# Kernel optimization log

Hardware: AMD Instinct MI355X
Metric: run time of the kernel (lower is better)

Reference implementation:

```python
import jax, jax.numpy as jnp
import numpy as np

GROUPS = 32
EPS = 1e-5


def _group_norm(x, w, b):
    B, C, H, W = x.shape
    xr = x.reshape(B, GROUPS, C // GROUPS, H, W)
    mean = xr.mean(axis=(2, 3, 4), keepdims=True)
    var = xr.var(axis=(2, 3, 4), keepdims=True)
    xn = ((xr - mean) * jax.lax.rsqrt(var + EPS)).reshape(B, C, H, W)
    return xn * w[None, :, None, None] + b[None, :, None, None]


def _conv1x1(w, b, x):
    # 1x1 conv == per-pixel channel matmul
    return jnp.einsum('oc,bchw->bohw', w, x) + b[None, :, None, None]


def setup_inputs() -> dict:
    key = jax.random.key(0)
    ks = jax.random.split(key, 6)
    C = 512
    s = 1.0 / np.sqrt(C)  # kaiming-uniform-ish scale for 1x1 convs
    return {
        'x': jax.random.normal(ks[0], (4, C, 64, 64), jnp.float32),
        'gn_w': jnp.ones((C,), jnp.float32),
        'gn_b': jnp.zeros((C,), jnp.float32),
        'qw': jax.random.normal(ks[1], (C, C), jnp.float32) * s,
        'qb': jnp.zeros((C,), jnp.float32),
        'kw': jax.random.normal(ks[2], (C, C), jnp.float32) * s,
        'kb': jnp.zeros((C,), jnp.float32),
        'vw': jax.random.normal(ks[3], (C, C), jnp.float32) * s,
        'vb': jnp.zeros((C,), jnp.float32),
        'pw': jax.random.normal(ks[4], (C, C), jnp.float32) * s,
        'pb': jnp.zeros((C,), jnp.float32),
    }


def reference(x, gn_w, gn_b, qw, qb, kw, kb, vw, vb, pw, pb):
    B, C, H, W = x.shape
    h_ = _group_norm(x, gn_w, gn_b)
    q = _conv1x1(qw, qb, h_).reshape(B, C, H * W)
    k = _conv1x1(kw, kb, h_).reshape(B, C, H * W)
    v = _conv1x1(vw, vb, h_).reshape(B, C, H * W)
    # scores [B, HW(query), HW(key)]
    scores = jnp.einsum('bcq,bck->bqk', q, k) * (C ** -0.5)
    attn = jax.nn.softmax(scores, axis=-1)
    out = jnp.einsum('bqk,bdk->bdq', attn, v).reshape(B, C, H, W)
    return x + _conv1x1(pw, pb, out)
```

## Files before the change

### kernel.cpp

```cpp
#include <hip/hip_runtime.h>

#define DEV __device__ __forceinline__

typedef __attribute__((ext_vector_type(8))) short short8;
typedef __attribute__((ext_vector_type(4))) float floatx4;
typedef __attribute__((ext_vector_type(4))) int i32x4;
typedef __attribute__((ext_vector_type(2))) long longx2;

DEV unsigned short f2bs(float x) {
    unsigned u = __float_as_uint(x);
    unsigned r = (u + 0x7fffu + ((u >> 16) & 1u)) >> 16;
    return (unsigned short)r;
}

DEV unsigned char f2fp8(float x) {
#if __has_builtin(__builtin_amdgcn_cvt_pk_fp8_f32)
    int pk = __builtin_amdgcn_cvt_pk_fp8_f32(x, 0.f, 0, false);
    return (unsigned char)(pk & 0xff);
#else
    unsigned u = __float_as_uint(x);
    unsigned s = (u >> 24) & 0x80;
    u &= 0x7fffffff;
    unsigned um = u + 0x7ffff + ((u >> 20) & 1);
    int e = (int)(um >> 23) - 120;
    unsigned char r;
    if (e <= 0) {
        float ax = __uint_as_float(u);
        int q = (int)rintf(ax * 512.f);
        r = (unsigned char)((q > 7) ? 8 : q);
    } else {
        r = (unsigned char)((e << 3) | ((um >> 20) & 7));
    }
    return r | s;
#endif
}

DEV unsigned pack_fp8x4(float v0, float v1, float v2, float v3) {
#if __has_builtin(__builtin_amdgcn_cvt_pk_fp8_f32)
    unsigned pk = (unsigned)__builtin_amdgcn_cvt_pk_fp8_f32(v0, v1, 0, false);
    pk = (unsigned)__builtin_amdgcn_cvt_pk_fp8_f32(v2, v3, (int)pk, true);
    return pk;
#else
    return (unsigned)f2fp8(v0) | ((unsigned)f2fp8(v1) << 8) |
           ((unsigned)f2fp8(v2) << 16) | ((unsigned)f2fp8(v3) << 24);
#endif
}

DEV unsigned pack_i8x4(float v0, float v1, float v2, float v3) {
    unsigned b0 = (unsigned)((int)rintf(v0)) & 255u;
    unsigned b1 = (unsigned)((int)rintf(v1)) & 255u;
    unsigned b2 = (unsigned)((int)rintf(v2)) & 255u;
    unsigned b3 = (unsigned)((int)rintf(v3)) & 255u;
    return b0 | (b1 << 8) | (b2 << 16) | (b3 << 24);
}

__global__ void gn_stats_kernel(const float* __restrict__ x, float* __restrict__ stats,
                                float* __restrict__ rowsum) {
    int bg = blockIdx.x;
    int tid = threadIdx.x;
    if (tid < 128) rowsum[bg * 128 + tid] = 0.f;
    const float4* p = (const float4*)(x + (size_t)bg * 65536);
    float s = 0.f, ss = 0.f;
    for (int i = tid; i < 16384; i += 256) {
        float4 v = p[i];
        s += v.x + v.y + v.z + v.w;
        ss += v.x * v.x + v.y * v.y + v.z * v.z + v.w * v.w;
    }
    for (int off = 32; off; off >>= 1) { s += __shfl_down(s, off); ss += __shfl_down(ss, off); }
    __shared__ float rs[4], rss[4];
    int wave = tid >> 6, lane = tid & 63;
    if (lane == 0) { rs[wave] = s; rss[wave] = ss; }
    __syncthreads();
    if (tid == 0) {
        float S = rs[0] + rs[1] + rs[2] + rs[3];
        float SS = rss[0] + rss[1] + rss[2] + rss[3];
        float mean = S * (1.f / 65536.f);
        float var = SS * (1.f / 65536.f) - mean * mean;
        stats[bg * 2] = mean;
        stats[bg * 2 + 1] = rsqrtf(var + 1e-5f);
    }
}

__global__ void gn_apply_kernel(const float* __restrict__ x, const float* __restrict__ stats,
                                const float* __restrict__ gw, const float* __restrict__ gb,
                                unsigned short* __restrict__ ht) {
    __shared__ __align__(16) unsigned short t[64][72];
    int b = blockIdx.z, c0 = blockIdx.y * 64, p0 = blockIdx.x * 64;
    int tid = threadIdx.x;
    const float* xb = x + ((size_t)b * 512 + c0) * 4096 + p0;
#pragma unroll
    for (int pass = 0; pass < 4; ++pass) {
        int cl = pass * 16 + (tid >> 4);
        int pq = (tid & 15) * 4;
        float4 v = *(const float4*)(xb + (size_t)cl * 4096 + pq);
        int c = c0 + cl, g = c >> 4;
        float mean = stats[(b * 32 + g) * 2], rstd = stats[(b * 32 + g) * 2 + 1];
        float sw = gw[c] * rstd;
        float sb = gb[c] - mean * sw;
        t[pq + 0][cl] = f2bs(v.x * sw + sb);
        t[pq + 1][cl] = f2bs(v.y * sw + sb);
        t[pq + 2][cl] = f2bs(v.z * sw + sb);
        t[pq + 3][cl] = f2bs(v.w * sw + sb);
    }
    __syncthreads();
    unsigned short* hb = ht + ((size_t)b * 4096 + p0) * 512 + c0;
#pragma unroll
    for (int pass = 0; pass < 2; ++pass) {
        int pl = pass * 32 + (tid >> 3);
        int c8 = (tid & 7) * 8;
        *(uint4*)(hb + (size_t)pl * 512 + c8) = *(const uint4*)&t[pl][c8];
    }
}

__global__ void cvt_bf16_kernel(const float* __restrict__ s, unsigned short* __restrict__ d, int n4) {
    int i = blockIdx.x * 256 + threadIdx.x;
    if (i >= n4) return;
    float4 v = ((const float4*)s)[i];
    ushort4 o;
    o.x = f2bs(v.x); o.y = f2bs(v.y); o.z = f2bs(v.z); o.w = f2bs(v.w);
    ((ushort4*)d)[i] = o;
}

template <int EPI>
__global__ void gemm_nt(const unsigned short* __restrict__ A, long long sAb,
                        const unsigned short* __restrict__ B, long long sBb,
                        void* __restrict__ Cv, void* __restrict__ Cv2, long long sCb,
                        const float* __restrict__ bias,
                        const float* __restrict__ resid, long long sRb,
                        int M, int N, int K, int Nst, int NS, float scale) {
    __shared__ __align__(16) unsigned short lA[128 * 64];
    __shared__ __align__(16) unsigned short lB[128 * 64];
    const int tid = threadIdx.x;
    const int wave = tid >> 6, lane = tid & 63;
    const int m0 = blockIdx.y * 128, n0 = blockIdx.x * 128, bz = blockIdx.z;
    const unsigned short* Ab = A + (size_t)bz * sAb;
    const unsigned short* Bb = B + (size_t)bz * sBb;

    floatx4 acc[4][4];
#pragma unroll
    for (int i = 0; i < 4; i++)
#pragma unroll
        for (int j = 0; j < 4; j++) acc[i][j] = (floatx4){0.f, 0.f, 0.f, 0.f};

    const int wm = (wave >> 1) * 64, wn = (wave & 1) * 64;
    const int quad = lane >> 4;
    const int lc = lane & 15;
    const int lc7 = lc & 7;

    const int nk = K >> 6;
    for (int kt = 0; kt < nk; ++kt) {
        const int kbase = kt * 64;
#pragma unroll
        for (int c = 0; c < 4; ++c) {
            int d = c * 256 + tid;
            int r = d >> 3;
            int kc = (d & 7) ^ (r & 7);
            const unsigned short* ga = Ab + (size_t)(m0 + r) * K + kbase + kc * 8;
            const unsigned short* gb = Bb + (size_t)(n0 + r) * K + kbase + kc * 8;
            __builtin_amdgcn_global_load_lds(
                (const __attribute__((address_space(1))) void*)ga,
                (__attribute__((address_space(3))) void*)&lA[(size_t)(c * 256 + wave * 64) * 8], 16, 0, 0);
            __builtin_amdgcn_global_load_lds(
                (const __attribute__((address_space(1))) void*)gb,
                (__attribute__((address_space(3))) void*)&lB[(size_t)(c * 256 + wave * 64) * 8], 16, 0, 0);
        }
        __syncthreads();
#pragma unroll
        for (int kk = 0; kk < 2; ++kk) {
            const int swz = ((kk * 4 + quad) ^ lc7) * 8;
            short8 af[4], bf[4];
#pragma unroll
            for (int i = 0; i < 4; i++)
                af[i] = *(const short8*)&lA[(size_t)(wm + i * 16 + lc) * 64 + swz];
#pragma unroll
            for (int j = 0; j < 4; j++)
                bf[j] = *(const short8*)&lB[(size_t)(wn + j * 16 + lc) * 64 + swz];
#pragma unroll
            for (int i = 0; i < 4; i++)
#pragma unroll
                for (int j = 0; j < 4; j++)
                    acc[i][j] = __builtin_amdgcn_mfma_f32_16x16x32_bf16(af[i], bf[j], acc[i][j], 0, 0, 0);
        }
        __syncthreads();
    }

    const int rowb = quad * 4;
#pragma unroll
    for (int i = 0; i < 4; i++) {
#pragma unroll
        for (int r = 0; r < 4; r++) {
            const int m = m0 + wm + i * 16 + rowb + r;
            if constexpr (EPI == 0) {
                float q[4];
#pragma unroll
                for (int j = 0; j < 4; j++) {
                    const int n = n0 + wn + j * 16 + lc;
                    q[j] = fminf(fmaxf((acc[i][j][r] + bias[n]) * scale, -127.f), 127.f);
                }
                const int col64 = n0 + wn;
                char* outp = (char*)((col64 < NS) ? Cv : Cv2);
                size_t idx = (size_t)bz * sCb + (size_t)m * Nst +
                             (col64 - ((col64 < NS) ? 0 : NS)) + lc * 4;
                *(unsigned*)(outp + idx) = pack_i8x4(q[0], q[1], q[2], q[3]);
            } else if constexpr (EPI == 5) {
                const float bm = bias[m];
                float q[4];
#pragma unroll
                for (int j = 0; j < 4; j++)
                    q[j] = fminf(fmaxf(acc[i][j][r] + bm, -448.f), 448.f);
                size_t idx = (size_t)bz * sCb + (size_t)m * Nst + n0 + wn + lc * 4;
                *(unsigned*)((char*)Cv + idx) = pack_fp8x4(q[0], q[1], q[2], q[3]);
            } else {
#pragma unroll
                for (int j = 0; j < 4; j++) {
                    const int n = n0 + wn + j * 16 + lc;
                    size_t idx = (size_t)bz * sCb + (size_t)m * Nst + n;
                    ((float*)Cv)[idx] = acc[i][j][r] + bias[m] +
                                        resid[(size_t)bz * sRb + (size_t)m * Nst + n];
                }
            }
        }
    }
}

__global__ void gemm_i8_exp(const char* __restrict__ A, long long sAb,
                            const char* __restrict__ B, long long sBb,
                            char* __restrict__ Cv, long long sCb,
                            float* __restrict__ rowsum,
                            int M, int N, int K, float scale2) {
    __shared__ __align__(16) char lA[128 * 128];
    __shared__ __align__(16) char lB[128 * 128];
    const int tid = threadIdx.x;
    const int wave = tid >> 6, lane = tid & 63;
    const int m0 = blockIdx.y * 128, n0 = blockIdx.x * 128, bz = blockIdx.z;
    const char* Ab = A + (size_t)bz * sAb;
    const char* Bb = B + (size_t)bz * sBb;

    i32x4 acc[4][4];
#pragma unroll
    for (int i = 0; i < 4; i++)
#pragma unroll
        for (int j = 0; j < 4; j++) acc[i][j] = (i32x4){0, 0, 0, 0};

    const int wm = (wave >> 1) * 64, wn = (wave & 1) * 64;
    const int quad = lane >> 4;
    const int lc = lane & 15;
    const int lc7 = lc & 7;

    const int nk = K >> 7;
    for (int kt = 0; kt < nk; ++kt) {
        const int kbase = kt * 128;
#pragma unroll
        for (int c = 0; c < 4; ++c) {
            int d = c * 256 + tid;
            int r = d >> 3;
            int kc = (d & 7) ^ (r & 7);
            const char* ga = Ab + (size_t)(m0 + r) * K + kbase + kc * 16;
            const char* gb = Bb + (size_t)(n0 + r) * K + kbase + kc * 16;
            __builtin_amdgcn_global_load_lds(
                (const __attribute__((address_space(1))) void*)ga,
                (__attribute__((address_space(3))) void*)&lA[(size_t)(c * 256 + wave * 64) * 16], 16, 0, 0);
            __builtin_amdgcn_global_load_lds(
                (const __attribute__((address_space(1))) void*)gb,
                (__attribute__((address_space(3))) void*)&lB[(size_t)(c * 256 + wave * 64) * 16], 16, 0, 0);
        }
        __syncthreads();
#pragma unroll
        for (int kk = 0; kk < 2; ++kk) {
            const int swz = ((kk * 4 + quad) ^ lc7) * 16;
            i32x4 af[4], bf[4];
#pragma unroll
            for (int i = 0; i < 4; i++)
                af[i] = *(const i32x4*)&lA[(size_t)(wm + i * 16 + lc) * 128 + swz];
#pragma unroll
            for (int j = 0; j < 4; j++)
                bf[j] = *(const i32x4*)&lB[(size_t)(wn + j * 16 + lc) * 128 + swz];
#pragma unroll
            for (int i = 0; i < 4; i++)
#pragma unroll
                for (int j = 0; j < 4; j++)
                    acc[i][j] = __builtin_amdgcn_mfma_i32_16x16x64_i8(af[i], bf[j], acc[i][j], 0, 0, 0);
        }
        __syncthreads();
    }

    const int rowb = quad * 4;
#pragma unroll
    for (int i = 0; i < 4; i++) {
#pragma unroll
        for (int r = 0; r < 4; r++) {
            const int m = m0 + wm + i * 16 + rowb + r;
            float e[4];
            float rsacc = 0.f;
#pragma unroll
            for (int j = 0; j < 4; j++) {
                e[j] = fminf(exp2f(fmaf((float)acc[i][j][r], scale2, -2.0f)), 448.f);
                rsacc += e[j];
            }
            size_t idx = (size_t)bz * sCb + (size_t)m * N + n0 + wn + lc * 4;
            *(unsigned*)(Cv + idx) = pack_fp8x4(e[0], e[1], e[2], e[3]);
            rsacc += __shfl_xor(rsacc, 1);
            rsacc += __shfl_xor(rsacc, 2);
            rsacc += __shfl_xor(rsacc, 4);
            rsacc += __shfl_xor(rsacc, 8);
            if (lc == 0) atomicAdd(&rowsum[(size_t)bz * M + m], rsacc);
        }
    }
}

__global__ void gemm_fp8_o(const char* __restrict__ A, long long sAb,
                           const char* __restrict__ B, long long sBb,
                           unsigned short* __restrict__ Cv, long long sCb,
                           const float* __restrict__ rowsum,
                           int M, int N, int K) {
    __shared__ __align__(16) char lA[128 * 128];
    __shared__ __align__(16) char lB[128 * 128];
    const int tid = threadIdx.x;
    const int wave = tid >> 6, lane = tid & 63;
    int flat = blockIdx.x;
    int xcd = flat & 7, idx = flat >> 3;
    int nt = idx & 3, si = idx >> 2;
    int stripe = xcd * 16 + si;
    const int m0 = (stripe & 31) * 128;
    const int n0 = nt * 128;
    const int bz = stripe >> 5;
    const char* Ab = A + (size_t)bz * sAb;
    const char* Bb = B + (size_t)bz * sBb;

    floatx4 acc[4][4];
#pragma unroll
    for (int i = 0; i < 4; i++)
#pragma unroll
        for (int j = 0; j < 4; j++) acc[i][j] = (floatx4){0.f, 0.f, 0.f, 0.f};

    const int wm = (wave >> 1) * 64, wn = (wave & 1) * 64;
    const int quad = lane >> 4;
    const int lc = lane & 15;
    const int lc7 = lc & 7;
    const int half = quad & 1;

    const int nk = K >> 7;
    for (int kt = 0; kt < nk; ++kt) {
        const int kbase = kt * 128;
#pragma unroll
        for (int c = 0; c < 4; ++c) {
            int d = c * 256 + tid;
            int r = d >> 3;
            int kc = (d & 7) ^ (r & 7);
            const char* ga = Ab + (size_t)(m0 + r) * K + kbase + kc * 16;
            const char* gb = Bb + (size_t)(n0 + r) * K + kbase + kc * 16;
            __builtin_amdgcn_global_load_lds(
                (const __attribute__((address_space(1))) void*)ga,
                (__attribute__((address_space(3))) void*)&lA[(size_t)(c * 256 + wave * 64) * 16], 16, 0, 0);
            __builtin_amdgcn_global_load_lds(
                (const __attribute__((address_space(1))) void*)gb,
                (__attribute__((address_space(3))) void*)&lB[(size_t)(c * 256 + wave * 64) * 16], 16, 0, 0);
        }
        __syncthreads();
#pragma unroll
        for (int t = 0; t < 4; ++t) {
            const int swz = ((2 * t + (quad >> 1)) ^ lc7) * 16;
            long a8[4], b8[4];
#pragma unroll
            for (int i = 0; i < 4; i++) {
                longx2 v = *(const longx2*)&lA[(size_t)(wm + i * 16 + lc) * 128 + swz];
                a8[i] = v[half];
            }
#pragma unroll
            for (int j = 0; j < 4; j++) {
                longx2 v = *(const longx2*)&lB[(size_t)(wn + j * 16 + lc) * 128 + swz];
                b8[j] = v[half];
            }
#pragma unroll
            for (int i = 0; i < 4; i++)
#pragma unroll
                for (int j = 0; j < 4; j++)
                    acc[i][j] = __builtin_amdgcn_mfma_f32_16x16x32_fp8_fp8(a8[i], b8[j], acc[i][j], 0, 0, 0);
        }
        __syncthreads();
    }

    const int rowb = quad * 4;
#pragma unroll
    for (int i = 0; i < 4; i++) {
#pragma unroll
        for (int r = 0; r < 4; r++) {
            const int m = m0 + wm + i * 16 + rowb + r;
            const float pscale = 1.f / rowsum[(size_t)bz * M + m];
#pragma unroll
            for (int j = 0; j < 4; j++) {
                const int n = n0 + wn + j * 16 + lc;
                Cv[(size_t)bz * sCb + (size_t)m * N + n] = f2bs(acc[i][j][r] * pscale);
            }
        }
    }
}

extern "C" void kernel_launch(void* const* d_in, const int* in_sizes, int n_in,
                              void* d_out, int out_size, void* d_ws, size_t ws_size,
                              hipStream_t stream) {
    (void)in_sizes; (void)n_in; (void)out_size; (void)ws_size;
    const float* x   = (const float*)d_in[0];
    const float* gnw = (const float*)d_in[1];
    const float* gnb = (const float*)d_in[2];
    const float* qw  = (const float*)d_in[3];
    const float* qb  = (const float*)d_in[4];
    const float* kw  = (const float*)d_in[5];
    const float* kb  = (const float*)d_in[6];
    const float* vw  = (const float*)d_in[7];
    const float* vb  = (const float*)d_in[8];
    const float* pw  = (const float*)d_in[9];
    const float* pb  = (const float*)d_in[10];
    float* out = (float*)d_out;

    char* ws = (char*)d_ws;
    unsigned short* h_t = (unsigned short*)(ws);
    unsigned short* o_t = h_t;
    char* q_i8 = (char*)(ws + (16ull << 20));
    char* k_i8 = (char*)(ws + (32ull << 20));
    char* v_f8 = (char*)(ws + (48ull << 20));
    unsigned short* wqkb = (unsigned short*)(ws + (64ull << 20));
    unsigned short* wvb = (unsigned short*)(ws + (65ull << 20));
    unsigned short* wpb = wvb + 262144;
    float* stats  = (float*)(ws + (66ull << 20));
    float* rowsum = (float*)(ws + (66ull << 20) + 65536);
    float* biasqk = (float*)(ws + (66ull << 20) + 131072);
    char* p_f8 = (char*)(ws + (67ull << 20));

    const long long sP  = 2097152;
    const long long sS  = 16777216;
    const int BIG = 1 << 30;
    const float QS = 16.f;
    const float SC = 0.044194173824159216f / (QS * QS);
    const float LOG2E = 1.4426950408889634f;

    cvt_bf16_kernel<<<256, 256, 0, stream>>>(qw, wqkb, 65536);
    cvt_bf16_kernel<<<256, 256, 0, stream>>>(kw, wqkb + 262144, 65536);
    cvt_bf16_kernel<<<256, 256, 0, stream>>>(vw, wvb, 65536);
    cvt_bf16_kernel<<<256, 256, 0, stream>>>(pw, wpb, 65536);
    hipMemcpyAsync(biasqk, qb, 512 * sizeof(float), hipMemcpyDeviceToDevice, stream);
    hipMemcpyAsync(biasqk + 512, kb, 512 * sizeof(float), hipMemcpyDeviceToDevice, stream);
    gn_stats_kernel<<<128, 256, 0, stream>>>(x, stats, rowsum);
    gn_apply_kernel<<<dim3(64, 8, 4), 256, 0, stream>>>(x, stats, gnw, gnb, h_t);
    gemm_nt<0><<<dim3(8, 32, 4), 256, 0, stream>>>(h_t, sP, wqkb, 0, q_i8, k_i8, sP, biasqk,
                                                   nullptr, 0, 4096, 1024, 512, 512, 512, QS);
    gemm_nt<5><<<dim3(32, 4, 4), 256, 0, stream>>>(wvb, 0, h_t, sP, v_f8, v_f8, sP, vb,
                                                   nullptr, 0, 512, 4096, 512, 4096, BIG, 1.f);
    gemm_i8_exp<<<dim3(32, 32, 4), 256, 0, stream>>>(q_i8, sP, k_i8, sP, p_f8, sS, rowsum,
                                                     4096, 4096, 512, SC * LOG2E);
    gemm_fp8_o<<<dim3(512, 1, 1), 256, 0, stream>>>(p_f8, sS, v_f8, sP, o_t, sP, rowsum,
                                                    4096, 512, 4096);
    gemm_nt<4><<<dim3(32, 4, 4), 256, 0, stream>>>(wpb, 0, o_t, sP, (void*)out, nullptr, sP, pb,
                                                   x, sP, 512, 4096, 512, 4096, BIG, 1.f);
}
```

Measured before the change: 324.9 us.

## Merge setup launches, swizzle QK grid per XCD, vectorize output stores

```diff
diff --git a/kernel.cpp b/kernel.cpp
--- a/kernel.cpp
+++ b/kernel.cpp
@@ -20,18 +20,10 @@
 #else
     unsigned u = __float_as_uint(x);
     unsigned s = (u >> 24) & 0x80;
-    u &= 0x7fffffff;
-    unsigned um = u + 0x7ffff + ((u >> 20) & 1);
-    int e = (int)(um >> 23) - 120;
-    unsigned char r;
-    if (e <= 0) {
-        float ax = __uint_as_float(u);
-        int q = (int)rintf(ax * 512.f);
-        r = (unsigned char)((q > 7) ? 8 : q);
-    } else {
-        r = (unsigned char)((e << 3) | ((um >> 20) & 7));
-    }
-    return r | s;
+    unsigned a = u & 0x7fffffff;
+    unsigned um = a + 0x7ffffu + ((a >> 20) & 1u);
+    unsigned r = (a >= 0x3c800000u) ? ((um >> 20) - 0x3C0u) : 0u;
+    return (unsigned char)(r | s);
 #endif
 }
 
@@ -54,11 +46,47 @@
     return b0 | (b1 << 8) | (b2 << 16) | (b3 << 24);
 }
 
-__global__ void gn_stats_kernel(const float* __restrict__ x, float* __restrict__ stats,
-                                float* __restrict__ rowsum) {
+__global__ void setup_kernel(const float* __restrict__ qw, const float* __restrict__ kw,
+                             const float* __restrict__ vw, const float* __restrict__ pw,
+                             const float* __restrict__ qb, const float* __restrict__ kb,
+                             unsigned short* __restrict__ wqkb, unsigned short* __restrict__ wvb,
+                             unsigned short* __restrict__ wpb,
+                             float* __restrict__ biasqk, float* __restrict__ rowsum) {
+    int b = blockIdx.x, tid = threadIdx.x;
+    if (b < 768) {
+        const float* src = (b < 256) ? qw : (b < 512) ? kw : vw;
+        unsigned short* dst = (b < 256) ? wqkb : (b < 512) ? (wqkb + 262144) : wvb;
+        int off = (b & 255) * 256 + tid;
+        float4 v = ((const float4*)src)[off];
+        ushort4 o;
+        o.x = f2bs(v.x); o.y = f2bs(v.y); o.z = f2bs(v.z); o.w = f2bs(v.w);
+        ((ushort4*)dst)[off] = o;
+    } else if (b < 1024) {
+        int off = (b - 768) * 256 + tid;
+        int row = off >> 7, c4 = (off & 127) * 4;
+        float4 v = ((const float4*)pw)[off];
+        float vv[4] = {v.x, v.y, v.z, v.w};
+#pragma unroll
+        for (int e = 0; e < 4; ++e) {
+            int c = c4 + e;
+            int j = (c >> 4) & 3, lc = c & 15;
+            int cp = (c & ~63) | (lc * 4 + j);
+            wpb[row * 512 + cp] = f2bs(vv[e]);
+        }
+    } else {
+        biasqk[tid]       = qb[tid];
+        biasqk[256 + tid] = qb[256 + tid];
+        biasqk[512 + tid] = kb[tid];
+        biasqk[768 + tid] = kb[256 + tid];
+        float4 z = {0.f, 0.f, 0.f, 0.f};
+#pragma unroll
+        for (int k = 0; k < 16; ++k) ((float4*)rowsum)[k * 256 + tid] = z;
+    }
+}
+
+__global__ void gn_stats_kernel(const float* __restrict__ x, float* __restrict__ stats) {
     int bg = blockIdx.x;
     int tid = threadIdx.x;
-    if (tid < 128) rowsum[bg * 128 + tid] = 0.f;
     const float4* p = (const float4*)(x + (size_t)bg * 65536);
     float s = 0.f, ss = 0.f;
     for (int i = tid; i < 16384; i += 256) {
@@ -110,15 +138,6 @@
         int c8 = (tid & 7) * 8;
         *(uint4*)(hb + (size_t)pl * 512 + c8) = *(const uint4*)&t[pl][c8];
     }
-}
-
-__global__ void cvt_bf16_kernel(const float* __restrict__ s, unsigned short* __restrict__ d, int n4) {
-    int i = blockIdx.x * 256 + threadIdx.x;
-    if (i >= n4) return;
-    float4 v = ((const float4*)s)[i];
-    ushort4 o;
-    o.x = f2bs(v.x); o.y = f2bs(v.y); o.z = f2bs(v.z); o.w = f2bs(v.w);
-    ((ushort4*)d)[i] = o;
 }
 
 template <int EPI>
@@ -232,7 +251,13 @@
     __shared__ __align__(16) char lB[128 * 128];
     const int tid = threadIdx.x;
     const int wave = tid >> 6, lane = tid & 63;
-    const int m0 = blockIdx.y * 128, n0 = blockIdx.x * 128, bz = blockIdx.z;
+    const int flat = blockIdx.x;
+    const int xcd = flat & 7;
+    const int idx = flat >> 3;
+    const int bz = idx >> 7;
+    const int r2 = idx & 127;
+    const int m0 = (xcd * 4 + (r2 >> 5)) * 128;
+    const int n0 = (r2 & 31) * 128;
     const char* Ab = A + (size_t)bz * sAb;
     const char* Bb = B + (size_t)bz * sBb;
 
@@ -297,8 +322,8 @@
                 e[j] = fminf(exp2f(fmaf((float)acc[i][j][r], scale2, -2.0f)), 448.f);
                 rsacc += e[j];
             }
-            size_t idx = (size_t)bz * sCb + (size_t)m * N + n0 + wn + lc * 4;
-            *(unsigned*)(Cv + idx) = pack_fp8x4(e[0], e[1], e[2], e[3]);
+            size_t oidx = (size_t)bz * sCb + (size_t)m * N + n0 + wn + lc * 4;
+            *(unsigned*)(Cv + oidx) = pack_fp8x4(e[0], e[1], e[2], e[3]);
             rsacc += __shfl_xor(rsacc, 1);
             rsacc += __shfl_xor(rsacc, 2);
             rsacc += __shfl_xor(rsacc, 4);
@@ -387,11 +412,13 @@
         for (int r = 0; r < 4; r++) {
             const int m = m0 + wm + i * 16 + rowb + r;
             const float pscale = 1.f / rowsum[(size_t)bz * M + m];
-#pragma unroll
-            for (int j = 0; j < 4; j++) {
-                const int n = n0 + wn + j * 16 + lc;
-                Cv[(size_t)bz * sCb + (size_t)m * N + n] = f2bs(acc[i][j][r] * pscale);
-            }
+            unsigned short h[4];
+#pragma unroll
+            for (int j = 0; j < 4; j++) h[j] = f2bs(acc[i][j][r] * pscale);
+            uint2 u;
+            u.x = (unsigned)h[0] | ((unsigned)h[1] << 16);
+            u.y = (unsigned)h[2] | ((unsigned)h[3] << 16);
+            *(uint2*)&Cv[(size_t)bz * sCb + (size_t)m * N + n0 + wn + lc * 4] = u;
         }
     }
 }
@@ -434,20 +461,15 @@
     const float SC = 0.044194173824159216f / (QS * QS);
     const float LOG2E = 1.4426950408889634f;
 
-    cvt_bf16_kernel<<<256, 256, 0, stream>>>(qw, wqkb, 65536);
-    cvt_bf16_kernel<<<256, 256, 0, stream>>>(kw, wqkb + 262144, 65536);
-    cvt_bf16_kernel<<<256, 256, 0, stream>>>(vw, wvb, 65536);
-    cvt_bf16_kernel<<<256, 256, 0, stream>>>(pw, wpb, 65536);
-    hipMemcpyAsync(biasqk, qb, 512 * sizeof(float), hipMemcpyDeviceToDevice, stream);
-    hipMemcpyAsync(biasqk + 512, kb, 512 * sizeof(float), hipMemcpyDeviceToDevice, stream);
-    gn_stats_kernel<<<128, 256, 0, stream>>>(x, stats, rowsum);
+    setup_kernel<<<1025, 256, 0, stream>>>(qw, kw, vw, pw, qb, kb, wqkb, wvb, wpb, biasqk, rowsum);
+    gn_stats_kernel<<<128, 256, 0, stream>>>(x, stats);
     gn_apply_kernel<<<dim3(64, 8, 4), 256, 0, stream>>>(x, stats, gnw, gnb, h_t);
     gemm_nt<0><<<dim3(8, 32, 4), 256, 0, stream>>>(h_t, sP, wqkb, 0, q_i8, k_i8, sP, biasqk,
                                                    nullptr, 0, 4096, 1024, 512, 512, 512, QS);
     gemm_nt<5><<<dim3(32, 4, 4), 256, 0, stream>>>(wvb, 0, h_t, sP, v_f8, v_f8, sP, vb,
                                                    nullptr, 0, 512, 4096, 512, 4096, BIG, 1.f);
-    gemm_i8_exp<<<dim3(32, 32, 4), 256, 0, stream>>>(q_i8, sP, k_i8, sP, p_f8, sS, rowsum,
-                                                     4096, 4096, 512, SC * LOG2E);
+    gemm_i8_exp<<<dim3(4096, 1, 1), 256, 0, stream>>>(q_i8, sP, k_i8, sP, p_f8, sS, rowsum,
+                                                      4096, 4096, 512, SC * LOG2E);
     gemm_fp8_o<<<dim3(512, 1, 1), 256, 0, stream>>>(p_f8, sS, v_f8, sP, o_t, sP, rowsum,
                                                     4096, 512, 4096);
     gemm_nt<4><<<dim3(32, 4, 4), 256, 0, stream>>>(wpb, 0, o_t, sP, (void*)out, nullptr, sP, pb,
```

Result: faster. 314.2 us (-3.3%).
